# Kernel optimization log

Hardware: AMD Instinct MI355X
Metric: run time of the kernel (lower is better)

Reference implementation:

```python
import jax, jax.numpy as jnp
import numpy as np

B, T, D, H, E, K = 8, 1024, 1024, 16, 8, 2
HS = D // H  # head size
LN_EPS = 1e-5


def setup_inputs() -> dict:
    key = jax.random.key(0)
    ks = jax.random.split(key, 12)
    s = 0.02
    return {
        "x":  jax.random.normal(ks[0], (B, T, D), jnp.float32),
        "Wq": jax.random.normal(ks[1], (H, D, HS), jnp.float32) * s,
        "Wk": jax.random.normal(ks[2], (H, D, HS), jnp.float32) * s,
        "Wv": jax.random.normal(ks[3], (H, D, HS), jnp.float32) * s,
        "Wg": jax.random.normal(ks[4], (D, E), jnp.float32) * s,
        "W1": jax.random.normal(ks[5], (E, D, 4 * D), jnp.float32) * s,
        "b1": jnp.zeros((E, 4 * D), jnp.float32),
        "W2": jax.random.normal(ks[6], (E, 4 * D, D), jnp.float32) * s,
        "b2": jnp.zeros((E, D), jnp.float32),
        "g1": jnp.ones((D,), jnp.float32),
        "be1": jnp.zeros((D,), jnp.float32),
        "g2": jnp.ones((D,), jnp.float32),
        "be2": jnp.zeros((D,), jnp.float32),
    }


def _layernorm(h, g, b):
    mu = jnp.mean(h, axis=-1, keepdims=True)
    var = jnp.mean(jnp.square(h - mu), axis=-1, keepdims=True)
    return (h - mu) * jax.lax.rsqrt(var + LN_EPS) * g + b


def _attention(x, Wq, Wk, Wv):
    # per-head projections (no bias)
    q = jnp.einsum('btd,hde->bhte', x, Wq)
    k = jnp.einsum('btd,hde->bhte', x, Wk)
    v = jnp.einsum('btd,hde->bhte', x, Wv)
    # NOTE: original scales by C**-0.5 where C = x.shape[-1] = n_embed
    scores = jnp.einsum('bhte,bhse->bhts', q, k) * (D ** -0.5)
    causal = jnp.tril(jnp.ones((T, T), bool))
    scores = jnp.where(causal, scores, -jnp.inf)
    attn = jax.nn.softmax(scores, axis=-1)  # dropout = identity (eval)
    out = jnp.einsum('bhts,bhse->bhte', attn, v)
    # concat heads: [B,H,T,HS] -> [B,T,H*HS]
    return out.transpose(0, 2, 1, 3).reshape(B, T, D)


def _moe(x, Wg, W1, b1, W2, b2):
    xs = x.reshape(-1, D)                       # [N, D]
    logits = xs @ Wg                            # [N, E]
    w, sel = jax.lax.top_k(logits, K)           # [N, K]
    w = jax.nn.softmax(w.astype(jnp.float32), axis=-1).astype(x.dtype)
    # combine per-token per-expert weight: [N, E]
    we = jnp.sum(w[..., None] * (sel[..., None] == jnp.arange(E)), axis=1)
    res = jnp.zeros_like(xs)
    for e in range(E):  # fixed small expert count
        h = jax.nn.relu(xs @ W1[e] + b1[e])     # [N, 4D]
        y = h @ W2[e] + b2[e]                   # [N, D]
        res = res + we[:, e:e + 1] * y
    return res.reshape(x.shape)


def reference(x, Wq, Wk, Wv, Wg, W1, b1, W2, b2, g1, be1, g2, be2):
    out = x + _layernorm(_attention(x, Wq, Wk, Wv), g1, be1)
    out = out + _layernorm(_moe(x, Wg, W1, b1, W2, b2), g2, be2)
    return out
```

## Files before the change

### kernel.cpp

```cpp
#include <hip/hip_runtime.h>

#define B_    8
#define T_    1024
#define D_    1024
#define H_    16
#define HS_   64
#define E_    8
#define DFF   4096
#define NTOK  8192
#define NROW  16384

typedef unsigned short u16;
typedef unsigned int   u32;
typedef __attribute__((ext_vector_type(8))) short bf8;
typedef __attribute__((ext_vector_type(4))) float f4;

__device__ __forceinline__ u16 f2bf(float f) {
  u32 u = __float_as_uint(f);
  u32 r = (u + 0x7FFFu + ((u >> 16) & 1u)) >> 16;
  return (u16)r;
}
__device__ __forceinline__ float bf2f(u16 h) {
  return __uint_as_float(((u32)h) << 16);
}

__device__ __forceinline__ f4 mfma16(bf8 a, bf8 b, f4 c) {
  return __builtin_amdgcn_mfma_f32_16x16x32_bf16(a, b, c, 0, 0, 0);
}

typedef const __attribute__((address_space(1))) void* gas_ptr;
typedef __attribute__((address_space(3))) void* las_ptr;
__device__ __forceinline__ void async16(const void* g, void* l) {
  __builtin_amdgcn_global_load_lds((gas_ptr)g, (las_ptr)l, 16, 0, 0);
}

__device__ __forceinline__ void bar() {
  asm volatile("" ::: "memory");
  __builtin_amdgcn_s_barrier();
  asm volatile("" ::: "memory");
}

__global__ __launch_bounds__(256) void cvt_x_kernel(const float* __restrict__ x,
                                                    u16* __restrict__ xbf) {
  int i = blockIdx.x * 256 + threadIdx.x;
  float4 v = ((const float4*)x)[i];
  ushort4 o;
  o.x = f2bf(v.x); o.y = f2bf(v.y); o.z = f2bf(v.z); o.w = f2bf(v.w);
  ((ushort4*)xbf)[i] = o;
}

__global__ __launch_bounds__(256) void transpose_cvt_kernel(
    const float* __restrict__ src, u16* __restrict__ dst,
    int R, int C, size_t sStride, size_t dStride) {
  __shared__ float t[32][33];
  src += (size_t)blockIdx.z * sStride;
  dst += (size_t)blockIdx.z * dStride;
  int r0 = blockIdx.x * 32, c0 = blockIdx.y * 32;
  int tx = threadIdx.x & 31, ty = threadIdx.x >> 5;
#pragma unroll
  for (int i = 0; i < 32; i += 8)
    t[ty + i][tx] = src[(size_t)(r0 + ty + i) * C + (c0 + tx)];
  __syncthreads();
#pragma unroll
  for (int i = 0; i < 32; i += 8)
    dst[(size_t)(c0 + ty + i) * R + (r0 + tx)] = f2bf(t[tx][ty + i]);
}

__global__ __launch_bounds__(256) void vtrans_kernel(const u16* __restrict__ qkv,
                                                     u16* __restrict__ Vt) {
  __shared__ u16 t[32][33];
  int bh = blockIdx.z, b = bh >> 4, h = bh & 15;
  const u16* Vg = qkv + (size_t)(32 + h) * NTOK * HS_ + (size_t)b * T_ * HS_;
  u16* Vp = Vt + (size_t)bh * HS_ * T_;
  int t0 = blockIdx.x * 32, c0 = blockIdx.y * 32;
  int tx = threadIdx.x & 31, ty = threadIdx.x >> 5;
#pragma unroll
  for (int i = 0; i < 32; i += 8)
    t[ty + i][tx] = Vg[(size_t)(t0 + ty + i) * HS_ + c0 + tx];
  __syncthreads();
#pragma unroll
  for (int i = 0; i < 32; i += 8)
    Vp[(size_t)(c0 + ty + i) * T_ + t0 + tx] = t[tx][ty + i];
}

__global__ __launch_bounds__(256) void gating_kernel(
    const float* __restrict__ x, const float* __restrict__ Wg,
    int* __restrict__ sel, float* __restrict__ wgt) {
  int wave = threadIdx.x >> 6, lane = threadIdx.x & 63;
  int t = blockIdx.x * 4 + wave;
  int e = lane & 7, grp = lane >> 3;
  const float* xr = x + (size_t)t * D_;
  float acc = 0.f;
  for (int i = 0; i < 128; ++i) {
    int d = grp + i * 8;
    acc += xr[d] * Wg[d * 8 + e];
  }
  acc += __shfl_xor(acc, 8);
  acc += __shfl_xor(acc, 16);
  acc += __shfl_xor(acc, 32);
  float lg[8];
#pragma unroll
  for (int j = 0; j < 8; ++j) lg[j] = __shfl(acc, j);
  int s0 = 0; float v0 = lg[0];
#pragma unroll
  for (int j = 1; j < 8; ++j) if (lg[j] > v0) { v0 = lg[j]; s0 = j; }
  int s1 = -1; float v1 = -3.4e38f;
#pragma unroll
  for (int j = 0; j < 8; ++j) if (j != s0 && lg[j] > v1) { v1 = lg[j]; s1 = j; }
  if (lane == 0) {
    float dd = __expf(v1 - v0);
    float w0 = 1.f / (1.f + dd);
    sel[2 * t]     = s0; sel[2 * t + 1] = s1;
    wgt[2 * t]     = w0; wgt[2 * t + 1] = dd * w0;
  }
}

__global__ __launch_bounds__(256) void offsets_kernel(const int* __restrict__ sel,
                                                      int* __restrict__ meta) {
  __shared__ int hist[E_];
  int tid = threadIdx.x;
  if (tid < E_) hist[tid] = 0;
  __syncthreads();
  for (int i = tid; i < NROW; i += 256) atomicAdd(&hist[sel[i]], 1);
  __syncthreads();
  if (tid == 0) {
    int s = 0, mb = 0, mb2 = 0;
    for (int e = 0; e < E_; ++e) {
      int c = hist[e];
      meta[e] = c; meta[8 + e] = s; meta[16 + e] = mb; meta[32 + e] = mb2;
      s += c; mb += (c + 127) >> 7; mb2 += (c + 255) >> 8;
    }
    meta[24] = mb;
    meta[40] = mb2;
  }
}

__global__ __launch_bounds__(256) void assign_kernel(
    const int* __restrict__ sel, const float* __restrict__ wgt,
    const int* __restrict__ meta, int* __restrict__ gidx,
    float* __restrict__ gw, int* __restrict__ rowmap) {
  int e = blockIdx.x, tid = threadIdx.x, lane = tid & 63, wv = tid >> 6;
  __shared__ int wsum[4];
  __shared__ int carry;
  if (tid == 0) carry = meta[8 + e];
  __syncthreads();
  for (int base = 0; base < NROW; base += 256) {
    int idx = base + tid;
    int f = (sel[idx] == e) ? 1 : 0;
    unsigned long long mask = __ballot(f);
    int pre = __popcll(mask & ((1ull << lane) - 1ull));
    if (lane == 0) wsum[wv] = __popcll(mask);
    __syncthreads();
    int woff = 0;
    for (int w = 0; w < wv; ++w) woff += wsum[w];
    int cb = carry;
    if (f) {
      int pos = cb + woff + pre;
      gidx[pos] = idx >> 1;
      gw[pos] = wgt[idx];
      rowmap[idx] = pos;
    }
    __syncthreads();
    if (tid == 0) carry = cb + wsum[0] + wsum[1] + wsum[2] + wsum[3];
    __syncthreads();
  }
}

template <int MODE>
__global__ __launch_bounds__(512, 2) void gemm256(
    const u16* __restrict__ A, const u16* __restrict__ Bt,
    u16* __restrict__ outB, const float* __restrict__ bias,
    const int* __restrict__ meta, const int* __restrict__ gidx, int K) {
  int n0 = blockIdx.y * 256;
  int n_e = 0, off = 0, m0, e = 0;
  const u16* Ap = A;
  const u16* Bp = Bt;
  if constexpr (MODE != 0) {
    int xb = blockIdx.x;
#pragma unroll
    for (int j = 1; j < 8; ++j) if (meta[32 + j] <= xb) e = j;
    n_e = meta[e];
    off = meta[8 + e];
    m0 = (xb - meta[32 + e]) * 256;
    if (m0 >= n_e) return;
    if constexpr (MODE == 1) {
      Bp = Bt + (size_t)e * DFF * 1024;
    } else {
      Ap = A + (size_t)off * DFF;
      Bp = Bt + (size_t)e * 1024 * DFF;
    }
  } else {
    m0 = blockIdx.x * 256;
  }

  __shared__ __align__(16) u16 As[2][256 * 64];
  __shared__ __align__(16) u16 Bs[2][256 * 64];

  int tid = threadIdx.x, lane = tid & 63, w = tid >> 6;
  int wm = w >> 2, wn = w & 3;
  int ml = lane & 15, quad = lane >> 4;
  int lrow = lane >> 3;
  int gcol = ((lane & 7) ^ lrow) * 8;

  const u16* aptr[4];
  const u16* bptr[4];
#pragma unroll
  for (int i = 0; i < 4; ++i) {
    int ra = m0 + i * 64 + w * 8 + lrow;
    if constexpr (MODE == 1) {
      int rr = ra < n_e ? ra : n_e - 1;
      aptr[i] = Ap + (size_t)gidx[off + rr] * 1024 + gcol;
    } else if constexpr (MODE == 2) {
      int rr = ra < n_e ? ra : n_e - 1;
      aptr[i] = Ap + (size_t)rr * DFF + gcol;
    } else {
      aptr[i] = Ap + (size_t)ra * 1024 + gcol;
    }
    bptr[i] = Bp + (size_t)(n0 + i * 64 + w * 8 + lrow) * K + gcol;
  }

  const int NT = K >> 6;

  auto stA = [&](int buf, int t) {
#pragma unroll
    for (int i = 0; i < 4; ++i)
      async16(aptr[i] + t * 64, &As[buf][(i * 64 + w * 8) * 64]);
  };
  auto stB = [&](int buf, int t) {
#pragma unroll
    for (int i = 0; i < 4; ++i)
      async16(bptr[i] + t * 64, &Bs[buf][(i * 64 + w * 8) * 64]);
  };

  f4 acc[8][4];
#pragma unroll
  for (int i = 0; i < 8; ++i)
#pragma unroll
    for (int j = 0; j < 4; ++j) acc[i][j] = (f4){0.f, 0.f, 0.f, 0.f};

  stA(0, 0); stB(0, 0);
  stA(1, 1);
  asm volatile("s_waitcnt vmcnt(4)" ::: "memory");
  bar();

  int mq = ml & 7;
  bf8 af[8], bfr[4];

  for (int t = 0; t < NT; ++t) {
    const int c = t & 1;
    const u16* Ac = As[c];
    const u16* Bc = Bs[c];

#pragma unroll
    for (int mi = 0; mi < 8; ++mi)
      af[mi] = *(const bf8*)&Ac[(wm * 128 + mi * 16 + ml) * 64 + (quad ^ mq) * 8];
#pragma unroll
    for (int ni = 0; ni < 4; ++ni)
      bfr[ni] = *(const bf8*)&Bc[(wn * 64 + ni * 16 + ml) * 64 + (quad ^ mq) * 8];
    if (t + 1 < NT) stB(c ^ 1, t + 1);
    bar();
    __builtin_amdgcn_s_setprio(1);
#pragma unroll
    for (int mi = 0; mi < 8; ++mi) {
      acc[mi][0] = mfma16(af[mi], bfr[0], acc[mi][0]);
      acc[mi][1] = mfma16(af[mi], bfr[1], acc[mi][1]);
    }
    __builtin_amdgcn_s_setprio(0);
    bar();

    __builtin_amdgcn_s_setprio(1);
#pragma unroll
    for (int mi = 0; mi < 8; ++mi) {
      acc[mi][2] = mfma16(af[mi], bfr[2], acc[mi][2]);
      acc[mi][3] = mfma16(af[mi], bfr[3], acc[mi][3]);
    }
    __builtin_amdgcn_s_setprio(0);
    bar();

#pragma unroll
    for (int mi = 0; mi < 8; ++mi)
      af[mi] = *(const bf8*)&Ac[(wm * 128 + mi * 16 + ml) * 64 + ((4 + quad) ^ mq) * 8];
#pragma unroll
    for (int ni = 0; ni < 4; ++ni)
      bfr[ni] = *(const bf8*)&Bc[(wn * 64 + ni * 16 + ml) * 64 + ((4 + quad) ^ mq) * 8];
    bar();
    __builtin_amdgcn_s_setprio(1);
#pragma unroll
    for (int mi = 0; mi < 8; ++mi) {
      acc[mi][0] = mfma16(af[mi], bfr[0], acc[mi][0]);
      acc[mi][1] = mfma16(af[mi], bfr[1], acc[mi][1]);
    }
    __builtin_amdgcn_s_setprio(0);
    bar();

    if (t + 2 < NT) stA(c, t + 2);
    __builtin_amdgcn_s_setprio(1);
#pragma unroll
    for (int mi = 0; mi < 8; ++mi) {
      acc[mi][2] = mfma16(af[mi], bfr[2], acc[mi][2]);
      acc[mi][3] = mfma16(af[mi], bfr[3], acc[mi][3]);
    }
    __builtin_amdgcn_s_setprio(0);
    if (t + 1 < NT) {
      if (t + 2 < NT) {
        asm volatile("s_waitcnt vmcnt(4)" ::: "memory");
      } else {
        asm volatile("s_waitcnt vmcnt(0)" ::: "memory");
      }
    }
    bar();
  }

#pragma unroll
  for (int mi = 0; mi < 8; ++mi)
#pragma unroll
    for (int ni = 0; ni < 4; ++ni)
#pragma unroll
      for (int rg = 0; rg < 4; ++rg) {
        int m = m0 + wm * 128 + mi * 16 + quad * 4 + rg;
        int n = n0 + wn * 64 + ni * 16 + ml;
        float v = acc[mi][ni][rg];
        if constexpr (MODE == 0) {
          int pl = n >> 6, col = n & 63;
          outB[(size_t)pl * NTOK * HS_ + (size_t)m * HS_ + col] = f2bf(v);
        } else if constexpr (MODE == 1) {
          if (m < n_e) {
            float hv = v + bias[e * DFF + n];
            outB[(size_t)(off + m) * DFF + n] = f2bf(fmaxf(hv, 0.f));
          }
        } else {
          if (m < n_e) {
            outB[(size_t)(off + m) * 1024 + n] = f2bf(v + bias[e * 1024 + n]);
          }
        }
      }
}

__global__ __launch_bounds__(256) void attn_kernel(const u16* __restrict__ qkv,
                                                   const u16* __restrict__ Vt,
                                                   float* __restrict__ attn_out) {
  int qt = blockIdx.x, bh = blockIdx.y;
  int b = bh >> 4, h = bh & 15;
  int q0 = qt * 64;
  const u16* Qg = qkv + (size_t)h * NTOK * HS_ + (size_t)b * T_ * HS_;
  const u16* Kg = qkv + (size_t)(16 + h) * NTOK * HS_ + (size_t)b * T_ * HS_;
  const u16* Vp = Vt + (size_t)bh * HS_ * T_;
  __shared__ __align__(16) u16 Qs[64 * 72];
  __shared__ __align__(16) u16 Ks[64 * 72];
  __shared__ __align__(16) u16 Vs[64 * 72];
  __shared__ __align__(16) u16 Ps[64 * 72];
  int tid = threadIdx.x, lane = tid & 63, wave = tid >> 6;
  int ml = lane & 15, quad = lane >> 4;

  for (int i = tid; i < 512; i += 256) {
    int r = i >> 3, c = (i & 7) * 8;
    *(uint4*)&Qs[r * 72 + c] = *(const uint4*)(Qg + (size_t)(q0 + r) * HS_ + c);
  }

  f4 acc_o[4];
  float m_[4], l_[4];
#pragma unroll
  for (int i = 0; i < 4; ++i) {
    acc_o[i] = (f4){0.f, 0.f, 0.f, 0.f};
    m_[i] = -1e30f; l_[i] = 0.f;
  }

  for (int ck = 0; ck <= qt; ++ck) {
    int kv0 = ck * 64;
    __syncthreads();
    for (int i = tid; i < 512; i += 256) {
      int r = i >> 3, c = (i & 7) * 8;
      *(uint4*)&Ks[r * 72 + c] = *(const uint4*)(Kg + (size_t)(kv0 + r) * HS_ + c);
      *(uint4*)&Vs[r * 72 + c] = *(const uint4*)(Vp + (size_t)r * T_ + kv0 + c);
    }
    __syncthreads();

    f4 sacc[4];
#pragma unroll
    for (int nt = 0; nt < 4; ++nt) sacc[nt] = (f4){0.f, 0.f, 0.f, 0.f};
#pragma unroll
    for (int kk = 0; kk < 64; kk += 32) {
      bf8 a = *(const bf8*)&Qs[(wave * 16 + ml) * 72 + kk + quad * 8];
#pragma unroll
      for (int nt = 0; nt < 4; ++nt) {
        bf8 bk = *(const bf8*)&Ks[(nt * 16 + ml) * 72 + kk + quad * 8];
        sacc[nt] = mfma16(a, bk, sacc[nt]);
      }
    }

    bool dm = (kv0 == q0);
    float pv[4][4], mx[4];
#pragma unroll
    for (int rg = 0; rg < 4; ++rg) {
      int gq = q0 + wave * 16 + quad * 4 + rg;
      float mm = -1e30f;
#pragma unroll
      for (int nt = 0; nt < 4; ++nt) {
        float s = sacc[nt][rg] * 0.03125f;
        if (dm && (kv0 + nt * 16 + ml) > gq) s = -1e30f;
        pv[nt][rg] = s;
        mm = fmaxf(mm, s);
      }
      mx[rg] = mm;
    }
#pragma unroll
    for (int off = 1; off < 16; off <<= 1)
#pragma unroll
      for (int rg = 0; rg < 4; ++rg) mx[rg] = fmaxf(mx[rg], __shfl_xor(mx[rg], off));

    float al[4], rs[4];
#pragma unroll
    for (int rg = 0; rg < 4; ++rg) {
      float mn = fmaxf(m_[rg], mx[rg]);
      al[rg] = __expf(m_[rg] - mn);
      m_[rg] = mn;
      float r = 0.f;
#pragma unroll
      for (int nt = 0; nt < 4; ++nt) {
        float ev = __expf(pv[nt][rg] - mn);
        pv[nt][rg] = ev;
        r += ev;
      }
      rs[rg] = r;
    }
#pragma unroll
    for (int off = 1; off < 16; off <<= 1)
#pragma unroll
      for (int rg = 0; rg < 4; ++rg) rs[rg] += __shfl_xor(rs[rg], off);

#pragma unroll
    for (int rg = 0; rg < 4; ++rg) {
      l_[rg] = al[rg] * l_[rg] + rs[rg];
#pragma unroll
      for (int nt = 0; nt < 4; ++nt) {
        acc_o[nt][rg] *= al[rg];
        Ps[(wave * 16 + quad * 4 + rg) * 72 + nt * 16 + ml] = f2bf(pv[nt][rg]);
      }
    }

#pragma unroll
    for (int kk = 0; kk < 64; kk += 32) {
      bf8 a = *(const bf8*)&Ps[(wave * 16 + ml) * 72 + kk + quad * 8];
#pragma unroll
      for (int ci = 0; ci < 4; ++ci) {
        bf8 bv = *(const bf8*)&Vs[(ci * 16 + ml) * 72 + kk + quad * 8];
        acc_o[ci] = mfma16(a, bv, acc_o[ci]);
      }
    }
  }

#pragma unroll
  for (int rg = 0; rg < 4; ++rg) {
    float inv = 1.f / l_[rg];
    int gq = q0 + wave * 16 + quad * 4 + rg;
    float* orow = attn_out + (size_t)(b * T_ + gq) * D_ + h * HS_;
#pragma unroll
    for (int ci = 0; ci < 4; ++ci) orow[ci * 16 + ml] = acc_o[ci][rg] * inv;
  }
}

__global__ __launch_bounds__(256) void final_kernel(
    const float* __restrict__ x, const float* __restrict__ attn,
    const u16* __restrict__ Y, const int* __restrict__ rowmap,
    const float* __restrict__ wgt,
    const float* __restrict__ g1, const float* __restrict__ be1,
    const float* __restrict__ g2, const float* __restrict__ be2,
    float* __restrict__ out) {
  int t = blockIdx.x, tid = threadIdx.x;
  int lane = tid & 63, wave = tid >> 6;
  float4 av = ((const float4*)(attn + (size_t)t * D_))[tid];
  int r0 = rowmap[2 * t], r1 = rowmap[2 * t + 1];
  float w0 = wgt[2 * t], w1 = wgt[2 * t + 1];
  ushort4 y0 = ((const ushort4*)(Y + (size_t)r0 * D_))[tid];
  ushort4 y1 = ((const ushort4*)(Y + (size_t)r1 * D_))[tid];
  float4 mv;
  mv.x = w0 * bf2f(y0.x) + w1 * bf2f(y1.x);
  mv.y = w0 * bf2f(y0.y) + w1 * bf2f(y1.y);
  mv.z = w0 * bf2f(y0.z) + w1 * bf2f(y1.z);
  mv.w = w0 * bf2f(y0.w) + w1 * bf2f(y1.w);

  float sa = av.x + av.y + av.z + av.w;
  float qa = av.x * av.x + av.y * av.y + av.z * av.z + av.w * av.w;
  float sm = mv.x + mv.y + mv.z + mv.w;
  float qm = mv.x * mv.x + mv.y * mv.y + mv.z * mv.z + mv.w * mv.w;
#pragma unroll
  for (int off = 1; off < 64; off <<= 1) {
    sa += __shfl_xor(sa, off);
    qa += __shfl_xor(qa, off);
    sm += __shfl_xor(sm, off);
    qm += __shfl_xor(qm, off);
  }
  __shared__ float red[4][4];
  if (lane == 0) { red[wave][0] = sa; red[wave][1] = qa; red[wave][2] = sm; red[wave][3] = qm; }
  __syncthreads();
  sa = red[0][0] + red[1][0] + red[2][0] + red[3][0];
  qa = red[0][1] + red[1][1] + red[2][1] + red[3][1];
  sm = red[0][2] + red[1][2] + red[2][2] + red[3][2];
  qm = red[0][3] + red[1][3] + red[2][3] + red[3][3];
  const float inv_d = 1.f / 1024.f;
  float mu1 = sa * inv_d, var1 = qa * inv_d - mu1 * mu1;
  float mu2 = sm * inv_d, var2 = qm * inv_d - mu2 * mu2;
  float rs1 = rsqrtf(var1 + 1e-5f), rs2 = rsqrtf(var2 + 1e-5f);

  float4 xv = ((const float4*)(x + (size_t)t * D_))[tid];
  float4 g1v = ((const float4*)g1)[tid], b1v = ((const float4*)be1)[tid];
  float4 g2v = ((const float4*)g2)[tid], b2v = ((const float4*)be2)[tid];
  float4 o;
  o.x = xv.x + (av.x - mu1) * rs1 * g1v.x + b1v.x + (mv.x - mu2) * rs2 * g2v.x + b2v.x;
  o.y = xv.y + (av.y - mu1) * rs1 * g1v.y + b1v.y + (mv.y - mu2) * rs2 * g2v.y + b2v.y;
  o.z = xv.z + (av.z - mu1) * rs1 * g1v.z + b1v.z + (mv.z - mu2) * rs2 * g2v.z + b2v.z;
  o.w = xv.w + (av.w - mu1) * rs1 * g1v.w + b1v.w + (mv.w - mu2) * rs2 * g2v.w + b2v.w;
  ((float4*)(out + (size_t)t * D_))[tid] = o;
}

extern "C" void kernel_launch(void* const* d_in, const int* in_sizes, int n_in,
                              void* d_out, int out_size, void* d_ws, size_t ws_size,
                              hipStream_t stream) {
  const float* x   = (const float*)d_in[0];
  const float* Wq  = (const float*)d_in[1];
  const float* Wk  = (const float*)d_in[2];
  const float* Wv  = (const float*)d_in[3];
  const float* Wg  = (const float*)d_in[4];
  const float* W1  = (const float*)d_in[5];
  const float* b1  = (const float*)d_in[6];
  const float* W2  = (const float*)d_in[7];
  const float* b2  = (const float*)d_in[8];
  const float* g1  = (const float*)d_in[9];
  const float* be1 = (const float*)d_in[10];
  const float* g2  = (const float*)d_in[11];
  const float* be2 = (const float*)d_in[12];
  float* out = (float*)d_out;

  char* ws = (char*)d_ws;
  size_t off = 0;
  auto alloc = [&](size_t bytes) -> void* {
    void* p = ws + off;
    off = (off + bytes + 255) & ~(size_t)255;
    return p;
  };
  u16*   xbf    = (u16*)alloc((size_t)NTOK * D_ * 2);
  u16*   wqkvt  = (u16*)alloc((size_t)48 * 64 * 1024 * 2);
  u16*   w1t    = (u16*)alloc((size_t)E_ * DFF * 1024 * 2);
  u16*   w2t    = (u16*)alloc((size_t)E_ * 1024 * DFF * 2);
  u16*   qkv    = (u16*)alloc((size_t)48 * NTOK * HS_ * 2);
  float* attn   = (float*)alloc((size_t)NTOK * D_ * 4);
  u16*   Hbuf   = (u16*)alloc((size_t)NROW * DFF * 2);
  u16*   Ybuf   = (u16*)alloc((size_t)NROW * 1024 * 2);
  int*   meta   = (int*)alloc(256);
  int*   sel    = (int*)alloc(NROW * 4);
  float* wgt    = (float*)alloc(NROW * 4);
  int*   gidx   = (int*)alloc(NROW * 4);
  float* gw     = (float*)alloc(NROW * 4);
  int*   rowmap = (int*)alloc(NROW * 4);
  u16*   Vt     = Hbuf;
  (void)ws_size; (void)in_sizes; (void)n_in; (void)out_size; (void)gw;

  cvt_x_kernel<<<NTOK * D_ / 1024, 256, 0, stream>>>(x, xbf);
  transpose_cvt_kernel<<<dim3(32, 2, 16), 256, 0, stream>>>(Wq, wqkvt, 1024, 64, 65536, 65536);
  transpose_cvt_kernel<<<dim3(32, 2, 16), 256, 0, stream>>>(Wk, wqkvt + 16 * 65536, 1024, 64, 65536, 65536);
  transpose_cvt_kernel<<<dim3(32, 2, 16), 256, 0, stream>>>(Wv, wqkvt + 32 * 65536, 1024, 64, 65536, 65536);
  transpose_cvt_kernel<<<dim3(32, 128, 8), 256, 0, stream>>>(W1, w1t, 1024, 4096, (size_t)1024 * 4096, (size_t)1024 * 4096);
  transpose_cvt_kernel<<<dim3(128, 32, 8), 256, 0, stream>>>(W2, w2t, 4096, 1024, (size_t)4096 * 1024, (size_t)4096 * 1024);

  gating_kernel<<<NTOK / 4, 256, 0, stream>>>(x, Wg, sel, wgt);
  offsets_kernel<<<1, 256, 0, stream>>>(sel, meta);
  assign_kernel<<<E_, 256, 0, stream>>>(sel, wgt, meta, gidx, gw, rowmap);

  gemm256<0><<<dim3(32, 12), 512, 0, stream>>>(xbf, wqkvt, qkv, nullptr, nullptr, nullptr, 1024);
  vtrans_kernel<<<dim3(32, 2, 128), 256, 0, stream>>>(qkv, Vt);
  attn_kernel<<<dim3(16, 128), 256, 0, stream>>>(qkv, Vt, attn);

  gemm256<1><<<dim3(72, 16), 512, 0, stream>>>(xbf, w1t, Hbuf, b1, meta, gidx, 1024);
  gemm256<2><<<dim3(72, 4), 512, 0, stream>>>(Hbuf, w2t, Ybuf, b2, meta, gidx, 4096);

  final_kernel<<<NTOK, 256, 0, stream>>>(x, attn, Ybuf, rowmap, wgt, g1, be1, g2, be2, out);
}
```

Before: 1.191 ms.

## Replace 8-wave ping-pong GEMM schedule with simple double-buffered loop

The hand-tuned schedule, which interleaved barriers with s_setprio and staggered A/B prefetches under explicit vmcnt waits, is replaced by a plain double-buffered loop. Each tile issues the next tile's async loads, runs all MFMAs for both K-halves, then does one __syncthreads. The launch bound drops its min-blocks-per-CU hint, and the shared buffers become separate named arrays. This cuts barrier count and code complexity, but it gives up the cooperative wave scheduling and finer load/compute overlap, and it relies on __syncthreads to cover completion of the async LDS loads.

Result: faster. 1.113 ms (-6.5%).

```diff
diff --git a/kernel.cpp b/kernel.cpp
--- a/kernel.cpp
+++ b/kernel.cpp
@@ -32,12 +32,6 @@
 typedef __attribute__((address_space(3))) void* las_ptr;
 __device__ __forceinline__ void async16(const void* g, void* l) {
   __builtin_amdgcn_global_load_lds((gas_ptr)g, (las_ptr)l, 16, 0, 0);
-}
-
-__device__ __forceinline__ void bar() {
-  asm volatile("" ::: "memory");
-  __builtin_amdgcn_s_barrier();
-  asm volatile("" ::: "memory");
 }
 
 __global__ __launch_bounds__(256) void cvt_x_kernel(const float* __restrict__ x,
@@ -167,7 +161,7 @@
 }
 
 template <int MODE>
-__global__ __launch_bounds__(512, 2) void gemm256(
+__global__ __launch_bounds__(512) void gemm256(
     const u16* __restrict__ A, const u16* __restrict__ Bt,
     u16* __restrict__ outB, const float* __restrict__ bias,
     const int* __restrict__ meta, const int* __restrict__ gidx, int K) {
@@ -193,8 +187,10 @@
     m0 = blockIdx.x * 256;
   }
 
-  __shared__ __align__(16) u16 As[2][256 * 64];
-  __shared__ __align__(16) u16 Bs[2][256 * 64];
+  __shared__ __align__(16) u16 As0[256 * 64];
+  __shared__ __align__(16) u16 As1[256 * 64];
+  __shared__ __align__(16) u16 Bs0[256 * 64];
+  __shared__ __align__(16) u16 Bs1[256 * 64];
 
   int tid = threadIdx.x, lane = tid & 63, w = tid >> 6;
   int wm = w >> 2, wn = w & 3;
@@ -220,17 +216,7 @@
   }
 
   const int NT = K >> 6;
-
-  auto stA = [&](int buf, int t) {
-#pragma unroll
-    for (int i = 0; i < 4; ++i)
-      async16(aptr[i] + t * 64, &As[buf][(i * 64 + w * 8) * 64]);
-  };
-  auto stB = [&](int buf, int t) {
-#pragma unroll
-    for (int i = 0; i < 4; ++i)
-      async16(bptr[i] + t * 64, &Bs[buf][(i * 64 + w * 8) * 64]);
-  };
+  int mq = ml & 7;
 
   f4 acc[8][4];
 #pragma unroll
@@ -238,77 +224,51 @@
 #pragma unroll
     for (int j = 0; j < 4; ++j) acc[i][j] = (f4){0.f, 0.f, 0.f, 0.f};
 
-  stA(0, 0); stB(0, 0);
-  stA(1, 1);
-  asm volatile("s_waitcnt vmcnt(4)" ::: "memory");
-  bar();
-
-  int mq = ml & 7;
-  bf8 af[8], bfr[4];
-
-  for (int t = 0; t < NT; ++t) {
-    const int c = t & 1;
-    const u16* Ac = As[c];
-    const u16* Bc = Bs[c];
-
+  auto do_tile = [&](const u16* __restrict__ Ac, const u16* __restrict__ Bc,
+                     u16* __restrict__ An, u16* __restrict__ Bn, int tn) {
+    bf8 af[8], bfr[4];
 #pragma unroll
     for (int mi = 0; mi < 8; ++mi)
       af[mi] = *(const bf8*)&Ac[(wm * 128 + mi * 16 + ml) * 64 + (quad ^ mq) * 8];
 #pragma unroll
     for (int ni = 0; ni < 4; ++ni)
       bfr[ni] = *(const bf8*)&Bc[(wn * 64 + ni * 16 + ml) * 64 + (quad ^ mq) * 8];
-    if (t + 1 < NT) stB(c ^ 1, t + 1);
-    bar();
-    __builtin_amdgcn_s_setprio(1);
-#pragma unroll
-    for (int mi = 0; mi < 8; ++mi) {
-      acc[mi][0] = mfma16(af[mi], bfr[0], acc[mi][0]);
-      acc[mi][1] = mfma16(af[mi], bfr[1], acc[mi][1]);
-    }
-    __builtin_amdgcn_s_setprio(0);
-    bar();
-
-    __builtin_amdgcn_s_setprio(1);
-#pragma unroll
-    for (int mi = 0; mi < 8; ++mi) {
-      acc[mi][2] = mfma16(af[mi], bfr[2], acc[mi][2]);
-      acc[mi][3] = mfma16(af[mi], bfr[3], acc[mi][3]);
-    }
-    __builtin_amdgcn_s_setprio(0);
-    bar();
-
+    if (tn < NT) {
+#pragma unroll
+      for (int i = 0; i < 4; ++i)
+        async16(aptr[i] + tn * 64, &An[(i * 64 + w * 8) * 64]);
+#pragma unroll
+      for (int i = 0; i < 4; ++i)
+        async16(bptr[i] + tn * 64, &Bn[(i * 64 + w * 8) * 64]);
+    }
+#pragma unroll
+    for (int mi = 0; mi < 8; ++mi)
+#pragma unroll
+      for (int ni = 0; ni < 4; ++ni)
+        acc[mi][ni] = mfma16(af[mi], bfr[ni], acc[mi][ni]);
 #pragma unroll
     for (int mi = 0; mi < 8; ++mi)
       af[mi] = *(const bf8*)&Ac[(wm * 128 + mi * 16 + ml) * 64 + ((4 + quad) ^ mq) * 8];
 #pragma unroll
     for (int ni = 0; ni < 4; ++ni)
       bfr[ni] = *(const bf8*)&Bc[(wn * 64 + ni * 16 + ml) * 64 + ((4 + quad) ^ mq) * 8];
-    bar();
-    __builtin_amdgcn_s_setprio(1);
-#pragma unroll
-    for (int mi = 0; mi < 8; ++mi) {
-      acc[mi][0] = mfma16(af[mi], bfr[0], acc[mi][0]);
-      acc[mi][1] = mfma16(af[mi], bfr[1], acc[mi][1]);
-    }
-    __builtin_amdgcn_s_setprio(0);
-    bar();
-
-    if (t + 2 < NT) stA(c, t + 2);
-    __builtin_amdgcn_s_setprio(1);
-#pragma unroll
-    for (int mi = 0; mi < 8; ++mi) {
-      acc[mi][2] = mfma16(af[mi], bfr[2], acc[mi][2]);
-      acc[mi][3] = mfma16(af[mi], bfr[3], acc[mi][3]);
-    }
-    __builtin_amdgcn_s_setprio(0);
-    if (t + 1 < NT) {
-      if (t + 2 < NT) {
-        asm volatile("s_waitcnt vmcnt(4)" ::: "memory");
-      } else {
-        asm volatile("s_waitcnt vmcnt(0)" ::: "memory");
-      }
-    }
-    bar();
+#pragma unroll
+    for (int mi = 0; mi < 8; ++mi)
+#pragma unroll
+      for (int ni = 0; ni < 4; ++ni)
+        acc[mi][ni] = mfma16(af[mi], bfr[ni], acc[mi][ni]);
+    __syncthreads();
+  };
+
+#pragma unroll
+  for (int i = 0; i < 4; ++i) async16(aptr[i], &As0[(i * 64 + w * 8) * 64]);
+#pragma unroll
+  for (int i = 0; i < 4; ++i) async16(bptr[i], &Bs0[(i * 64 + w * 8) * 64]);
+  __syncthreads();
+
+  for (int t = 0; t < NT; t += 2) {
+    do_tile(As0, Bs0, As1, Bs1, t + 1);
+    do_tile(As1, Bs1, As0, Bs0, t + 2);
   }
 
 #pragma unroll
```
